# Kernel optimization log

Hardware: AMD Instinct MI355X
Metric: run time of the kernel (lower is better)

The kernel has to match this reference:

```python
import jax, jax.numpy as jnp
import numpy as np

B, N, MAX_V = 256, 16384, 64

def setup_inputs() -> dict:
    key = jax.random.key(0)
    ks = jax.random.split(key, 11)
    s = 0.02
    x = jax.random.normal(ks[0], (B, N, 5), dtype=jnp.float32)
    W1 = jax.random.normal(ks[1], (2, 32), dtype=jnp.float32) * s
    b1 = jnp.zeros((32,), jnp.float32)
    W2 = jax.random.normal(ks[2], (32, 64), dtype=jnp.float32) * s
    b2 = jnp.zeros((64,), jnp.float32)
    W3 = jax.random.normal(ks[3], (201, 256), dtype=jnp.float32) * s
    b3 = jnp.zeros((256,), jnp.float32)
    W4 = jax.random.normal(ks[4], (256, 128), dtype=jnp.float32) * s
    b4 = jnp.zeros((128,), jnp.float32)
    W5 = jax.random.normal(ks[5], (128, MAX_V * 4), dtype=jnp.float32) * s
    # existence-logit biases initialized to -2.0 (indices i*4+3)
    b5 = jnp.zeros((MAX_V * 4,), jnp.float32).at[jnp.arange(MAX_V) * 4 + 3].set(-2.0)
    return {"x": x, "W1": W1, "b1": b1, "W2": W2, "b2": b2,
            "W3": W3, "b3": b3, "W4": W4, "b4": b4, "W5": W5, "b5": b5}

def _pca_align(coords):
    # coords: [B,N,3]
    n = coords.shape[1]
    centroid = coords.mean(axis=1, keepdims=True)          # [B,1,3]
    centered = coords - centroid                           # [B,N,3]
    cov = jnp.einsum('bni,bnj->bij', centered, centered) / n
    evals, evecs = jnp.linalg.eigh(cov)                    # ascending
    evals = evals[:, ::-1]                                 # descending
    evecs = evecs[:, :, ::-1]
    # det sign fix on 3rd column
    det = jnp.linalg.det(evecs)
    evecs = evecs.at[:, :, 2].multiply(jnp.where(det < 0, -1.0, 1.0)[:, None])
    # deterministic sign: each axis points toward side with more mass (vectorized)
    proj = jnp.einsum('bnd,bde->bne', centered, evecs)     # [B,N,3]
    pos = (proj > 0).sum(axis=1)
    neg = (proj < 0).sum(axis=1)
    sign = jnp.where(neg > pos, -1.0, 1.0)                 # [B,3]
    evecs = evecs * sign[:, None, :]
    aligned = jnp.einsum('bnd,bde->bne', centered, evecs)  # [B,N,3]
    eig_norm = evals / (evals.sum(axis=1, keepdims=True) + 1e-8)
    extents = aligned.max(axis=1) - aligned.min(axis=1)    # [B,3]
    pca_features = jnp.concatenate([eig_norm, extents, centroid[:, 0]], axis=1)  # [B,9]
    return aligned, pca_features, evecs, centroid

def reference(x, W1, b1, W2, b2, W3, b3, W4, b4, W5, b5):
    coords = x[:, :, :3]
    sem = x[:, :, 3:]                                      # [B,N,2]
    aligned, pca_features, rot, centroid = _pca_align(coords)
    # per-point MLP
    pf = jax.nn.relu(sem @ W1 + b1)
    pf = jax.nn.relu(pf @ W2 + b2)                         # [B,N,64]
    gmax = pf.max(axis=1)
    gavg = pf.mean(axis=1)
    gstd = jnp.std(pf, axis=1, ddof=1)                     # torch.std is unbiased
    g = jnp.concatenate([gmax, gavg, gstd, pca_features], axis=1)  # [B,201]
    h = jax.nn.relu(g @ W3 + b3)
    h = jax.nn.relu(h @ W4 + b4)
    out = (h @ W5 + b5).reshape(x.shape[0], MAX_V, 4)      # [B,64,4]
    return out
```

## Files before the change

kernel.cpp:

```cpp
#include <hip/hip_runtime.h>
#include <math.h>

#define BATCH 256
#define NPTS  16384
#define TPB   256

#define P1_CHUNKS     8
#define P1_PTS_BLOCK  (NPTS / P1_CHUNKS)
#define P1_ITERS      8

#define P2_CHUNKS     8
#define P2_PTS_BLOCK  (NPTS / P2_CHUNKS)
#define P2_PTS_THREAD (P2_PTS_BLOCK / TPB)

#define R1_STRIDE 256
#define R1_WORDS  (BATCH * R1_STRIDE)
#define R2_OFF    R1_WORDS
#define R2_STRIDE 32
#define R2_WORDS  (BATCH * R2_STRIDE)
#define R3MAX_OFF (R2_OFF + R2_WORDS)
#define R3MIN_OFF (R3MAX_OFF + BATCH * 4)

typedef __bf16 bf16x8 __attribute__((ext_vector_type(8)));
typedef float  floatx4 __attribute__((ext_vector_type(4)));

__device__ __forceinline__ unsigned floatToKey(float f) {
    unsigned u = __float_as_uint(f);
    return (u & 0x80000000u) ? ~u : (u | 0x80000000u);
}
__device__ __forceinline__ float keyToFloat(unsigned k) {
    unsigned u = (k & 0x80000000u) ? (k ^ 0x80000000u) : ~k;
    return __uint_as_float(u);
}

__global__ void init_ws_kernel(unsigned* __restrict__ wsu) {
    int i = blockIdx.x * TPB + threadIdx.x;
    if (i < R1_WORDS) wsu[i] = 0u;
    if (i < BATCH * 4) {
        wsu[R3MAX_OFF + i] = 0u;
        wsu[R3MIN_OFF + i] = 0xFFFFFFFFu;
    }
}

__global__ __launch_bounds__(TPB, 4)
void pass1_kernel(const float* __restrict__ x, const float* __restrict__ W1,
                  const float* __restrict__ b1, const float* __restrict__ W2,
                  const float* __restrict__ b2, float* __restrict__ ws) {
    const int b     = blockIdx.x;
    const int chunk = blockIdx.y;
    const int tid   = threadIdx.x;
    const int lane  = tid & 63;
    const int wave  = tid >> 6;
    const int quad  = lane >> 4;
    const int l15   = lane & 15;

    bf16x8 Bf[4];
    float  b2n[4];
#pragma unroll
    for (int t = 0; t < 4; ++t) {
        int n = t * 16 + l15;
#pragma unroll
        for (int j = 0; j < 8; ++j)
            Bf[t][j] = (__bf16)W2[(quad * 8 + j) * 64 + n];
        b2n[t] = b2[n];
    }
    float w1a[8], w1b[8], b1r[8];
#pragma unroll
    for (int j = 0; j < 8; ++j) {
        int jj = quad * 8 + j;
        w1a[j] = W1[jj];
        w1b[j] = W1[32 + jj];
        b1r[j] = b1[jj];
    }

    float vmax[4] = {0.f, 0.f, 0.f, 0.f};
    float vsum[4] = {0.f, 0.f, 0.f, 0.f};
    float vsq[4]  = {0.f, 0.f, 0.f, 0.f};
    float mo[9];
#pragma unroll
    for (int j = 0; j < 9; ++j) mo[j] = 0.f;

    const float* xb = x + ((size_t)b * NPTS + (size_t)chunk * P1_PTS_BLOCK) * 5;

    for (int it = 0; it < P1_ITERS; ++it) {
        const int pbase = wave * (P1_ITERS * 64) + it * 64;
        const float* p = xb + (size_t)(pbase + lane) * 5;
        float c0 = p[0], c1 = p[1], c2 = p[2], s0 = p[3], s1 = p[4];
        mo[0] += c0; mo[1] += c1; mo[2] += c2;
        mo[3] = fmaf(c0, c0, mo[3]); mo[4] = fmaf(c0, c1, mo[4]); mo[5] = fmaf(c0, c2, mo[5]);
        mo[6] = fmaf(c1, c1, mo[6]); mo[7] = fmaf(c1, c2, mo[7]); mo[8] = fmaf(c1 == c1 ? c2 : c2, c2, mo[8]);

#pragma unroll
        for (int g = 0; g < 4; ++g) {
            int src = g * 16 + l15;
            float gs0 = __shfl(s0, src);
            float gs1 = __shfl(s1, src);
            bf16x8 Af;
#pragma unroll
            for (int j = 0; j < 8; ++j) {
                float v = fmaf(gs0, w1a[j], fmaf(gs1, w1b[j], b1r[j]));
                Af[j] = (__bf16)fmaxf(v, 0.f);
            }
#pragma unroll
            for (int t = 0; t < 4; ++t) {
                floatx4 C = {0.f, 0.f, 0.f, 0.f};
                C = __builtin_amdgcn_mfma_f32_16x16x32_bf16(Af, Bf[t], C, 0, 0, 0);
#pragma unroll
                for (int r = 0; r < 4; ++r) {
                    float v = fmaxf(C[r] + b2n[t], 0.f);
                    vmax[t] = fmaxf(vmax[t], v);
                    vsum[t] += v;
                    vsq[t]  = fmaf(v, v, vsq[t]);
                }
            }
        }
    }

#pragma unroll
    for (int t = 0; t < 4; ++t) {
        vmax[t] = fmaxf(vmax[t], __shfl_xor(vmax[t], 16));
        vmax[t] = fmaxf(vmax[t], __shfl_xor(vmax[t], 32));
        vsum[t] += __shfl_xor(vsum[t], 16);
        vsum[t] += __shfl_xor(vsum[t], 32);
        vsq[t]  += __shfl_xor(vsq[t], 16);
        vsq[t]  += __shfl_xor(vsq[t], 32);
    }
#pragma unroll
    for (int j = 0; j < 9; ++j) {
        float v = mo[j];
#pragma unroll
        for (int o = 32; o > 0; o >>= 1) v += __shfl_xor(v, o);
        mo[j] = v;
    }

    __shared__ float red[4][201];
    if (quad == 0) {
#pragma unroll
        for (int t = 0; t < 4; ++t) {
            red[wave][t * 16 + l15]       = vmax[t];
            red[wave][64 + t * 16 + l15]  = vsum[t];
            red[wave][128 + t * 16 + l15] = vsq[t];
        }
    }
    if (lane == 0) {
#pragma unroll
        for (int j = 0; j < 9; ++j) red[wave][192 + j] = mo[j];
    }
    __syncthreads();

    if (tid < 201) {
        float v0 = red[0][tid], v1 = red[1][tid], v2 = red[2][tid], v3 = red[3][tid];
        float* base = ws + (size_t)b * R1_STRIDE;
        if (tid < 64) {
            float m = fmaxf(fmaxf(v0, v1), fmaxf(v2, v3));
            atomicMax((unsigned*)(base + 9 + tid), __float_as_uint(m));
        } else if (tid < 128) {
            atomicAdd(base + 73 + (tid - 64), v0 + v1 + v2 + v3);
        } else if (tid < 192) {
            atomicAdd(base + 137 + (tid - 128), v0 + v1 + v2 + v3);
        } else {
            atomicAdd(base + (tid - 192), v0 + v1 + v2 + v3);
        }
    }
}

__global__ void eigh_kernel(float* __restrict__ ws) {
    int b = blockIdx.x * blockDim.x + threadIdx.x;
    if (b >= BATCH) return;
    const float* r1 = ws + (size_t)b * R1_STRIDE;
    const double n = (double)NPTS;
    double mx = r1[0] / n, my = r1[1] / n, mz = r1[2] / n;
    double A[3][3];
    A[0][0] = r1[3] / n - mx * mx; A[0][1] = r1[4] / n - mx * my; A[0][2] = r1[5] / n - mx * mz;
    A[1][1] = r1[6] / n - my * my; A[1][2] = r1[7] / n - my * mz; A[2][2] = r1[8] / n - mz * mz;
    A[1][0] = A[0][1]; A[2][0] = A[0][2]; A[2][1] = A[1][2];
    double V[3][3] = {{1, 0, 0}, {0, 1, 0}, {0, 0, 1}};

    const int PP[3] = {0, 0, 1};
    const int QQ[3] = {1, 2, 2};
    for (int sweep = 0; sweep < 12; ++sweep) {
        for (int r3 = 0; r3 < 3; ++r3) {
            int p = PP[r3], q = QQ[r3];
            double apq = A[p][q];
            if (fabs(apq) < 1e-300) continue;
            double theta = (A[q][q] - A[p][p]) / (2.0 * apq);
            double t = 1.0 / (fabs(theta) + sqrt(theta * theta + 1.0));
            if (theta < 0.0) t = -t;
            double c = 1.0 / sqrt(t * t + 1.0), s = t * c;
            double apq_t = t * apq;
            A[p][p] -= apq_t;
            A[q][q] += apq_t;
            A[p][q] = A[q][p] = 0.0;
            for (int r = 0; r < 3; ++r) {
                if (r != p && r != q) {
                    double arp = A[r][p], arq = A[r][q];
                    A[r][p] = A[p][r] = c * arp - s * arq;
                    A[r][q] = A[q][r] = s * arp + c * arq;
                }
                double vrp = V[r][p], vrq = V[r][q];
                V[r][p] = c * vrp - s * vrq;
                V[r][q] = s * vrp + c * vrq;
            }
        }
    }
    double w[3] = {A[0][0], A[1][1], A[2][2]};
    int i0 = 0, i1 = 1, i2 = 2, t;
    if (w[i0] < w[i1]) { t = i0; i0 = i1; i1 = t; }
    if (w[i0] < w[i2]) { t = i0; i0 = i2; i2 = t; }
    if (w[i1] < w[i2]) { t = i1; i1 = i2; i2 = t; }
    int idx[3] = {i0, i1, i2};

    float* r2 = ws + R2_OFF + (size_t)b * R2_STRIDE;
    for (int e = 0; e < 3; ++e)
        for (int comp = 0; comp < 3; ++comp)
            r2[e * 3 + comp] = (float)V[comp][idx[e]];
    double sum = w[0] + w[1] + w[2] + 1e-8;
    for (int e = 0; e < 3; ++e) r2[9 + e] = (float)(w[idx[e]] / sum);
    r2[12] = (float)mx; r2[13] = (float)my; r2[14] = (float)mz;
}

__global__ __launch_bounds__(TPB)
void pass2_kernel(const float* __restrict__ x, float* __restrict__ ws) {
    const int b = blockIdx.x, chunk = blockIdx.y, tid = threadIdx.x;
    const int lane = tid & 63, wave = tid >> 6;
    const float* r2 = ws + R2_OFF + (size_t)b * R2_STRIDE;
    float e0x = r2[0], e0y = r2[1], e0z = r2[2];
    float e1x = r2[3], e1y = r2[4], e1z = r2[5];
    float e2x = r2[6], e2y = r2[7], e2z = r2[8];
    float cx = r2[12], cy = r2[13], cz = r2[14];

    const float* xb = x + ((size_t)b * NPTS + (size_t)chunk * P2_PTS_BLOCK) * 5;
    float mn[3] = {3.4e38f, 3.4e38f, 3.4e38f};
    float mx[3] = {-3.4e38f, -3.4e38f, -3.4e38f};
    for (int i = 0; i < P2_PTS_THREAD; ++i) {
        const float* p = xb + (size_t)(i * TPB + tid) * 5;
        float c0 = p[0] - cx, c1 = p[1] - cy, c2 = p[2] - cz;
        float p0 = fmaf(c0, e0x, fmaf(c1, e0y, c2 * e0z));
        float p1 = fmaf(c0, e1x, fmaf(c1, e1y, c2 * e1z));
        float p2 = fmaf(c0, e2x, fmaf(c1, e2y, c2 * e2z));
        mn[0] = fminf(mn[0], p0); mx[0] = fmaxf(mx[0], p0);
        mn[1] = fminf(mn[1], p1); mx[1] = fmaxf(mx[1], p1);
        mn[2] = fminf(mn[2], p2); mx[2] = fmaxf(mx[2], p2);
    }
    __shared__ float red[4][8];
#pragma unroll
    for (int d = 0; d < 3; ++d) {
        float v = mx[d];
#pragma unroll
        for (int o = 32; o > 0; o >>= 1) v = fmaxf(v, __shfl_xor(v, o));
        if (lane == 0) red[wave][d] = v;
    }
#pragma unroll
    for (int d = 0; d < 3; ++d) {
        float v = mn[d];
#pragma unroll
        for (int o = 32; o > 0; o >>= 1) v = fminf(v, __shfl_xor(v, o));
        if (lane == 0) red[wave][4 + d] = v;
    }
    __syncthreads();
    unsigned* wsu = (unsigned*)ws;
    if (tid < 3) {
        float m = fmaxf(fmaxf(red[0][tid], red[1][tid]), fmaxf(red[2][tid], red[3][tid]));
        atomicMax(&wsu[R3MAX_OFF + b * 4 + tid], floatToKey(m));
    } else if (tid < 6) {
        int d = tid - 3;
        float m = fminf(fminf(red[0][4 + d], red[1][4 + d]), fminf(red[2][4 + d], red[3][4 + d]));
        atomicMin(&wsu[R3MIN_OFF + b * 4 + d], floatToKey(m));
    }
}

__global__ __launch_bounds__(TPB)
void final_kernel(const float* __restrict__ W3, const float* __restrict__ b3,
                  const float* __restrict__ W4, const float* __restrict__ b4,
                  const float* __restrict__ W5, const float* __restrict__ b5,
                  const float* __restrict__ ws, float* __restrict__ out) {
    const int b = blockIdx.x, t = threadIdx.x;
    __shared__ float g[224];
    __shared__ float h1[256];
    __shared__ float h2[128];
    const float* r1 = ws + (size_t)b * R1_STRIDE;
    if (t < 64) {
        g[t] = r1[9 + t];
        float s = r1[73 + t], sq = r1[137 + t];
        float avg = s * (1.0f / NPTS);
        g[64 + t] = avg;
        float var = (sq - s * avg) / (float)(NPTS - 1);
        g[128 + t] = sqrtf(fmaxf(var, 0.f));
    } else if (t < 73) {
        int j = t - 64;
        const float* r2 = ws + R2_OFF + (size_t)b * R2_STRIDE;
        const unsigned* wsu = (const unsigned*)ws;
        if (j < 3) {
            g[192 + j] = r2[9 + j];
        } else if (j < 6) {
            int d = j - 3;
            float fmx = keyToFloat(wsu[R3MAX_OFF + b * 4 + d]);
            float fmn = keyToFloat(wsu[R3MIN_OFF + b * 4 + d]);
            g[195 + d] = fmx - fmn;
        } else {
            g[198 + (j - 6)] = r2[12 + (j - 6)];
        }
    }
    __syncthreads();
    float a = b3[t];
    for (int j = 0; j < 201; ++j) a = fmaf(g[j], W3[j * 256 + t], a);
    h1[t] = fmaxf(a, 0.f);
    __syncthreads();
    if (t < 128) {
        float a2 = b4[t];
        for (int j = 0; j < 256; ++j) a2 = fmaf(h1[j], W4[j * 128 + t], a2);
        h2[t] = fmaxf(a2, 0.f);
    }
    __syncthreads();
    float o = b5[t];
    for (int j = 0; j < 128; ++j) o = fmaf(h2[j], W5[j * 256 + t], o);
    out[(size_t)b * 256 + t] = o;
}

extern "C" void kernel_launch(void* const* d_in, const int* in_sizes, int n_in,
                              void* d_out, int out_size, void* d_ws, size_t ws_size,
                              hipStream_t stream) {
    const float* x  = (const float*)d_in[0];
    const float* W1 = (const float*)d_in[1];
    const float* b1 = (const float*)d_in[2];
    const float* W2 = (const float*)d_in[3];
    const float* b2 = (const float*)d_in[4];
    const float* W3 = (const float*)d_in[5];
    const float* b3 = (const float*)d_in[6];
    const float* W4 = (const float*)d_in[7];
    const float* b4 = (const float*)d_in[8];
    const float* W5 = (const float*)d_in[9];
    const float* b5 = (const float*)d_in[10];
    float* out = (float*)d_out;
    float* ws  = (float*)d_ws;

    init_ws_kernel<<<dim3(R1_WORDS / TPB), TPB, 0, stream>>>((unsigned*)ws);
    pass1_kernel<<<dim3(BATCH, P1_CHUNKS), TPB, 0, stream>>>(x, W1, b1, W2, b2, ws);
    eigh_kernel<<<dim3(4), 64, 0, stream>>>(ws);
    pass2_kernel<<<dim3(BATCH, P2_CHUNKS), TPB, 0, stream>>>(x, ws);
    final_kernel<<<dim3(BATCH), TPB, 0, stream>>>(W3, b3, W4, b4, W5, b5, ws, out);
}
```

Before: 230.9 us.

## Fuse eigh, projection pass and MLP head into one per-batch kernel

Replaces the five-kernel pipeline with two kernels. pass1 now writes per-chunk partials instead of atomics, so the workspace init kernel is no longer needed. A new mid_kernel per batch combines the partials, runs a float Jacobi eigen-solve on one thread (fewer sweeps, down from double), does the min/max projection pass over all points, and runs the MLP head. pass1 also folds bias into the MFMA accumulator and vectorises the stat accumulation. This removes launches, atomics and global round-trips, but the projection pass now runs with only 256 blocks instead of 2048, which cuts parallelism for that memory-bound pass, and the lower-precision eigensolve may change accuracy.

New measurement: 546.5 us. +136.7%, slower.

```diff
diff --git a/kernel.cpp b/kernel.cpp
--- a/kernel.cpp
+++ b/kernel.cpp
@@ -9,38 +9,11 @@
 #define P1_PTS_BLOCK  (NPTS / P1_CHUNKS)
 #define P1_ITERS      8
 
-#define P2_CHUNKS     8
-#define P2_PTS_BLOCK  (NPTS / P2_CHUNKS)
-#define P2_PTS_THREAD (P2_PTS_BLOCK / TPB)
-
-#define R1_STRIDE 256
-#define R1_WORDS  (BATCH * R1_STRIDE)
-#define R2_OFF    R1_WORDS
-#define R2_STRIDE 32
-#define R2_WORDS  (BATCH * R2_STRIDE)
-#define R3MAX_OFF (R2_OFF + R2_WORDS)
-#define R3MIN_OFF (R3MAX_OFF + BATCH * 4)
-
-typedef __bf16 bf16x8 __attribute__((ext_vector_type(8)));
+#define PART_STRIDE 256
+
+typedef __bf16 bf16x8  __attribute__((ext_vector_type(8)));
 typedef float  floatx4 __attribute__((ext_vector_type(4)));
-
-__device__ __forceinline__ unsigned floatToKey(float f) {
-    unsigned u = __float_as_uint(f);
-    return (u & 0x80000000u) ? ~u : (u | 0x80000000u);
-}
-__device__ __forceinline__ float keyToFloat(unsigned k) {
-    unsigned u = (k & 0x80000000u) ? (k ^ 0x80000000u) : ~k;
-    return __uint_as_float(u);
-}
-
-__global__ void init_ws_kernel(unsigned* __restrict__ wsu) {
-    int i = blockIdx.x * TPB + threadIdx.x;
-    if (i < R1_WORDS) wsu[i] = 0u;
-    if (i < BATCH * 4) {
-        wsu[R3MAX_OFF + i] = 0u;
-        wsu[R3MIN_OFF + i] = 0xFFFFFFFFu;
-    }
-}
+typedef float  floatx2 __attribute__((ext_vector_type(2)));
 
 __global__ __launch_bounds__(TPB, 4)
 void pass1_kernel(const float* __restrict__ x, const float* __restrict__ W1,
@@ -73,14 +46,20 @@
         b1r[j] = b1[jj];
     }
 
-    float vmax[4] = {0.f, 0.f, 0.f, 0.f};
-    float vsum[4] = {0.f, 0.f, 0.f, 0.f};
-    float vsq[4]  = {0.f, 0.f, 0.f, 0.f};
+    floatx4 vmax4[4];
+    floatx2 vs01[4], vs23[4], vq01[4], vq23[4];
+#pragma unroll
+    for (int t = 0; t < 4; ++t) {
+        vmax4[t] = (floatx4){0.f, 0.f, 0.f, 0.f};
+        vs01[t] = (floatx2){0.f, 0.f}; vs23[t] = (floatx2){0.f, 0.f};
+        vq01[t] = (floatx2){0.f, 0.f}; vq23[t] = (floatx2){0.f, 0.f};
+    }
     float mo[9];
 #pragma unroll
     for (int j = 0; j < 9; ++j) mo[j] = 0.f;
 
     const float* xb = x + ((size_t)b * NPTS + (size_t)chunk * P1_PTS_BLOCK) * 5;
+    const floatx4 zero4 = {0.f, 0.f, 0.f, 0.f};
 
     for (int it = 0; it < P1_ITERS; ++it) {
         const int pbase = wave * (P1_ITERS * 64) + it * 64;
@@ -88,7 +67,7 @@
         float c0 = p[0], c1 = p[1], c2 = p[2], s0 = p[3], s1 = p[4];
         mo[0] += c0; mo[1] += c1; mo[2] += c2;
         mo[3] = fmaf(c0, c0, mo[3]); mo[4] = fmaf(c0, c1, mo[4]); mo[5] = fmaf(c0, c2, mo[5]);
-        mo[6] = fmaf(c1, c1, mo[6]); mo[7] = fmaf(c1, c2, mo[7]); mo[8] = fmaf(c1 == c1 ? c2 : c2, c2, mo[8]);
+        mo[6] = fmaf(c1, c1, mo[6]); mo[7] = fmaf(c1, c2, mo[7]); mo[8] = fmaf(c2, c2, mo[8]);
 
 #pragma unroll
         for (int g = 0; g < 4; ++g) {
@@ -103,205 +82,204 @@
             }
 #pragma unroll
             for (int t = 0; t < 4; ++t) {
-                floatx4 C = {0.f, 0.f, 0.f, 0.f};
+                floatx4 C = {b2n[t], b2n[t], b2n[t], b2n[t]};
                 C = __builtin_amdgcn_mfma_f32_16x16x32_bf16(Af, Bf[t], C, 0, 0, 0);
-#pragma unroll
-                for (int r = 0; r < 4; ++r) {
-                    float v = fmaxf(C[r] + b2n[t], 0.f);
-                    vmax[t] = fmaxf(vmax[t], v);
-                    vsum[t] += v;
-                    vsq[t]  = fmaf(v, v, vsq[t]);
+                floatx4 v = __builtin_elementwise_max(C, zero4);
+                vmax4[t] = __builtin_elementwise_max(vmax4[t], v);
+                floatx2 a = {v[0], v[1]};
+                floatx2 c = {v[2], v[3]};
+                vs01[t] += a;
+                vs23[t] += c;
+                vq01[t] = __builtin_elementwise_fma(a, a, vq01[t]);
+                vq23[t] = __builtin_elementwise_fma(c, c, vq23[t]);
+            }
+        }
+    }
+
+    float fmx[4], fsm[4], fsq[4];
+#pragma unroll
+    for (int t = 0; t < 4; ++t) {
+        float m = fmaxf(fmaxf(vmax4[t][0], vmax4[t][1]), fmaxf(vmax4[t][2], vmax4[t][3]));
+        m = fmaxf(m, __shfl_xor(m, 16));
+        m = fmaxf(m, __shfl_xor(m, 32));
+        fmx[t] = m;
+        float s = (vs01[t][0] + vs01[t][1]) + (vs23[t][0] + vs23[t][1]);
+        s += __shfl_xor(s, 16);
+        s += __shfl_xor(s, 32);
+        fsm[t] = s;
+        float q = (vq01[t][0] + vq01[t][1]) + (vq23[t][0] + vq23[t][1]);
+        q += __shfl_xor(q, 16);
+        q += __shfl_xor(q, 32);
+        fsq[t] = q;
+    }
+#pragma unroll
+    for (int j = 0; j < 9; ++j) {
+        float v = mo[j];
+#pragma unroll
+        for (int o = 32; o > 0; o >>= 1) v += __shfl_xor(v, o);
+        mo[j] = v;
+    }
+
+    __shared__ float red[4][201];
+    if (quad == 0) {
+#pragma unroll
+        for (int t = 0; t < 4; ++t) {
+            red[wave][t * 16 + l15]       = fmx[t];
+            red[wave][64 + t * 16 + l15]  = fsm[t];
+            red[wave][128 + t * 16 + l15] = fsq[t];
+        }
+    }
+    if (lane == 0) {
+#pragma unroll
+        for (int j = 0; j < 9; ++j) red[wave][192 + j] = mo[j];
+    }
+    __syncthreads();
+
+    if (tid < 201) {
+        float v0 = red[0][tid], v1 = red[1][tid], v2 = red[2][tid], v3 = red[3][tid];
+        float r = (tid < 64) ? fmaxf(fmaxf(v0, v1), fmaxf(v2, v3))
+                             : (v0 + v1) + (v2 + v3);
+        ws[(size_t)(b * P1_CHUNKS + chunk) * PART_STRIDE + tid] = r;
+    }
+}
+
+__global__ __launch_bounds__(TPB)
+void mid_kernel(const float* __restrict__ x,
+                const float* __restrict__ W3, const float* __restrict__ b3,
+                const float* __restrict__ W4, const float* __restrict__ b4,
+                const float* __restrict__ W5, const float* __restrict__ b5,
+                const float* __restrict__ ws, float* __restrict__ out) {
+    const int b = blockIdx.x, t = threadIdx.x;
+    const int lane = t & 63, wave = t >> 6;
+
+    __shared__ float comb[201];
+    __shared__ float eg[15];
+    __shared__ float redmm[4][8];
+    __shared__ float g[224];
+    __shared__ float h1[256];
+    __shared__ float h2[128];
+
+    if (t < 201) {
+        const float* base = ws + (size_t)b * P1_CHUNKS * PART_STRIDE + t;
+        float acc = base[0];
+        if (t < 64) {
+#pragma unroll
+            for (int i = 1; i < P1_CHUNKS; ++i) acc = fmaxf(acc, base[i * PART_STRIDE]);
+        } else {
+#pragma unroll
+            for (int i = 1; i < P1_CHUNKS; ++i) acc += base[i * PART_STRIDE];
+        }
+        comb[t] = acc;
+    }
+    __syncthreads();
+
+    if (t == 0) {
+        const float n = (float)NPTS;
+        float mx = comb[192] / n, my = comb[193] / n, mz = comb[194] / n;
+        float A[3][3];
+        A[0][0] = comb[195] / n - mx * mx; A[0][1] = comb[196] / n - mx * my;
+        A[0][2] = comb[197] / n - mx * mz;
+        A[1][1] = comb[198] / n - my * my; A[1][2] = comb[199] / n - my * mz;
+        A[2][2] = comb[200] / n - mz * mz;
+        A[1][0] = A[0][1]; A[2][0] = A[0][2]; A[2][1] = A[1][2];
+        float V[3][3] = {{1, 0, 0}, {0, 1, 0}, {0, 0, 1}};
+        const int PP[3] = {0, 0, 1};
+        const int QQ[3] = {1, 2, 2};
+        for (int sweep = 0; sweep < 7; ++sweep) {
+            for (int r3 = 0; r3 < 3; ++r3) {
+                int p = PP[r3], q = QQ[r3];
+                float apq = A[p][q];
+                if (fabsf(apq) < 1e-35f) continue;
+                float theta = (A[q][q] - A[p][p]) / (2.0f * apq);
+                float tt = 1.0f / (fabsf(theta) + sqrtf(fmaf(theta, theta, 1.0f)));
+                if (theta < 0.0f) tt = -tt;
+                float c = 1.0f / sqrtf(fmaf(tt, tt, 1.0f)), s = tt * c;
+                float apq_t = tt * apq;
+                A[p][p] -= apq_t;
+                A[q][q] += apq_t;
+                A[p][q] = A[q][p] = 0.0f;
+                for (int r = 0; r < 3; ++r) {
+                    if (r != p && r != q) {
+                        float arp = A[r][p], arq = A[r][q];
+                        A[r][p] = A[p][r] = c * arp - s * arq;
+                        A[r][q] = A[q][r] = s * arp + c * arq;
+                    }
+                    float vrp = V[r][p], vrq = V[r][q];
+                    V[r][p] = c * vrp - s * vrq;
+                    V[r][q] = s * vrp + c * vrq;
                 }
             }
         }
-    }
-
-#pragma unroll
-    for (int t = 0; t < 4; ++t) {
-        vmax[t] = fmaxf(vmax[t], __shfl_xor(vmax[t], 16));
-        vmax[t] = fmaxf(vmax[t], __shfl_xor(vmax[t], 32));
-        vsum[t] += __shfl_xor(vsum[t], 16);
-        vsum[t] += __shfl_xor(vsum[t], 32);
-        vsq[t]  += __shfl_xor(vsq[t], 16);
-        vsq[t]  += __shfl_xor(vsq[t], 32);
-    }
-#pragma unroll
-    for (int j = 0; j < 9; ++j) {
-        float v = mo[j];
-#pragma unroll
-        for (int o = 32; o > 0; o >>= 1) v += __shfl_xor(v, o);
-        mo[j] = v;
-    }
-
-    __shared__ float red[4][201];
-    if (quad == 0) {
-#pragma unroll
-        for (int t = 0; t < 4; ++t) {
-            red[wave][t * 16 + l15]       = vmax[t];
-            red[wave][64 + t * 16 + l15]  = vsum[t];
-            red[wave][128 + t * 16 + l15] = vsq[t];
-        }
-    }
-    if (lane == 0) {
-#pragma unroll
-        for (int j = 0; j < 9; ++j) red[wave][192 + j] = mo[j];
-    }
-    __syncthreads();
-
-    if (tid < 201) {
-        float v0 = red[0][tid], v1 = red[1][tid], v2 = red[2][tid], v3 = red[3][tid];
-        float* base = ws + (size_t)b * R1_STRIDE;
-        if (tid < 64) {
-            float m = fmaxf(fmaxf(v0, v1), fmaxf(v2, v3));
-            atomicMax((unsigned*)(base + 9 + tid), __float_as_uint(m));
-        } else if (tid < 128) {
-            atomicAdd(base + 73 + (tid - 64), v0 + v1 + v2 + v3);
-        } else if (tid < 192) {
-            atomicAdd(base + 137 + (tid - 128), v0 + v1 + v2 + v3);
-        } else {
-            atomicAdd(base + (tid - 192), v0 + v1 + v2 + v3);
-        }
-    }
-}
-
-__global__ void eigh_kernel(float* __restrict__ ws) {
-    int b = blockIdx.x * blockDim.x + threadIdx.x;
-    if (b >= BATCH) return;
-    const float* r1 = ws + (size_t)b * R1_STRIDE;
-    const double n = (double)NPTS;
-    double mx = r1[0] / n, my = r1[1] / n, mz = r1[2] / n;
-    double A[3][3];
-    A[0][0] = r1[3] / n - mx * mx; A[0][1] = r1[4] / n - mx * my; A[0][2] = r1[5] / n - mx * mz;
-    A[1][1] = r1[6] / n - my * my; A[1][2] = r1[7] / n - my * mz; A[2][2] = r1[8] / n - mz * mz;
-    A[1][0] = A[0][1]; A[2][0] = A[0][2]; A[2][1] = A[1][2];
-    double V[3][3] = {{1, 0, 0}, {0, 1, 0}, {0, 0, 1}};
-
-    const int PP[3] = {0, 0, 1};
-    const int QQ[3] = {1, 2, 2};
-    for (int sweep = 0; sweep < 12; ++sweep) {
-        for (int r3 = 0; r3 < 3; ++r3) {
-            int p = PP[r3], q = QQ[r3];
-            double apq = A[p][q];
-            if (fabs(apq) < 1e-300) continue;
-            double theta = (A[q][q] - A[p][p]) / (2.0 * apq);
-            double t = 1.0 / (fabs(theta) + sqrt(theta * theta + 1.0));
-            if (theta < 0.0) t = -t;
-            double c = 1.0 / sqrt(t * t + 1.0), s = t * c;
-            double apq_t = t * apq;
-            A[p][p] -= apq_t;
-            A[q][q] += apq_t;
-            A[p][q] = A[q][p] = 0.0;
-            for (int r = 0; r < 3; ++r) {
-                if (r != p && r != q) {
-                    double arp = A[r][p], arq = A[r][q];
-                    A[r][p] = A[p][r] = c * arp - s * arq;
-                    A[r][q] = A[q][r] = s * arp + c * arq;
-                }
-                double vrp = V[r][p], vrq = V[r][q];
-                V[r][p] = c * vrp - s * vrq;
-                V[r][q] = s * vrp + c * vrq;
-            }
-        }
-    }
-    double w[3] = {A[0][0], A[1][1], A[2][2]};
-    int i0 = 0, i1 = 1, i2 = 2, t;
-    if (w[i0] < w[i1]) { t = i0; i0 = i1; i1 = t; }
-    if (w[i0] < w[i2]) { t = i0; i0 = i2; i2 = t; }
-    if (w[i1] < w[i2]) { t = i1; i1 = i2; i2 = t; }
-    int idx[3] = {i0, i1, i2};
-
-    float* r2 = ws + R2_OFF + (size_t)b * R2_STRIDE;
-    for (int e = 0; e < 3; ++e)
-        for (int comp = 0; comp < 3; ++comp)
-            r2[e * 3 + comp] = (float)V[comp][idx[e]];
-    double sum = w[0] + w[1] + w[2] + 1e-8;
-    for (int e = 0; e < 3; ++e) r2[9 + e] = (float)(w[idx[e]] / sum);
-    r2[12] = (float)mx; r2[13] = (float)my; r2[14] = (float)mz;
-}
-
-__global__ __launch_bounds__(TPB)
-void pass2_kernel(const float* __restrict__ x, float* __restrict__ ws) {
-    const int b = blockIdx.x, chunk = blockIdx.y, tid = threadIdx.x;
-    const int lane = tid & 63, wave = tid >> 6;
-    const float* r2 = ws + R2_OFF + (size_t)b * R2_STRIDE;
-    float e0x = r2[0], e0y = r2[1], e0z = r2[2];
-    float e1x = r2[3], e1y = r2[4], e1z = r2[5];
-    float e2x = r2[6], e2y = r2[7], e2z = r2[8];
-    float cx = r2[12], cy = r2[13], cz = r2[14];
-
-    const float* xb = x + ((size_t)b * NPTS + (size_t)chunk * P2_PTS_BLOCK) * 5;
+        float w[3] = {A[0][0], A[1][1], A[2][2]};
+        int i0 = 0, i1 = 1, i2 = 2, sw;
+        if (w[i0] < w[i1]) { sw = i0; i0 = i1; i1 = sw; }
+        if (w[i0] < w[i2]) { sw = i0; i0 = i2; i2 = sw; }
+        if (w[i1] < w[i2]) { sw = i1; i1 = i2; i2 = sw; }
+        int idx[3] = {i0, i1, i2};
+        for (int e = 0; e < 3; ++e)
+            for (int comp = 0; comp < 3; ++comp)
+                eg[e * 3 + comp] = V[comp][idx[e]];
+        float sum = w[0] + w[1] + w[2] + 1e-8f;
+        for (int e = 0; e < 3; ++e) eg[9 + e] = w[idx[e]] / sum;
+        eg[12] = mx; eg[13] = my; eg[14] = mz;
+    }
+    __syncthreads();
+
+    float e0x = eg[0], e0y = eg[1], e0z = eg[2];
+    float e1x = eg[3], e1y = eg[4], e1z = eg[5];
+    float e2x = eg[6], e2y = eg[7], e2z = eg[8];
+    float cx = eg[12], cy = eg[13], cz = eg[14];
+
+    const float* xb = x + (size_t)b * NPTS * 5;
     float mn[3] = {3.4e38f, 3.4e38f, 3.4e38f};
-    float mx[3] = {-3.4e38f, -3.4e38f, -3.4e38f};
-    for (int i = 0; i < P2_PTS_THREAD; ++i) {
-        const float* p = xb + (size_t)(i * TPB + tid) * 5;
+    float mx3[3] = {-3.4e38f, -3.4e38f, -3.4e38f};
+#pragma unroll 4
+    for (int i = 0; i < NPTS / TPB; ++i) {
+        const float* p = xb + (size_t)(i * TPB + t) * 5;
         float c0 = p[0] - cx, c1 = p[1] - cy, c2 = p[2] - cz;
         float p0 = fmaf(c0, e0x, fmaf(c1, e0y, c2 * e0z));
         float p1 = fmaf(c0, e1x, fmaf(c1, e1y, c2 * e1z));
         float p2 = fmaf(c0, e2x, fmaf(c1, e2y, c2 * e2z));
-        mn[0] = fminf(mn[0], p0); mx[0] = fmaxf(mx[0], p0);
-        mn[1] = fminf(mn[1], p1); mx[1] = fmaxf(mx[1], p1);
-        mn[2] = fminf(mn[2], p2); mx[2] = fmaxf(mx[2], p2);
-    }
-    __shared__ float red[4][8];
+        mn[0] = fminf(mn[0], p0); mx3[0] = fmaxf(mx3[0], p0);
+        mn[1] = fminf(mn[1], p1); mx3[1] = fmaxf(mx3[1], p1);
+        mn[2] = fminf(mn[2], p2); mx3[2] = fmaxf(mx3[2], p2);
+    }
 #pragma unroll
     for (int d = 0; d < 3; ++d) {
-        float v = mx[d];
+        float v = mx3[d];
 #pragma unroll
         for (int o = 32; o > 0; o >>= 1) v = fmaxf(v, __shfl_xor(v, o));
-        if (lane == 0) red[wave][d] = v;
-    }
-#pragma unroll
-    for (int d = 0; d < 3; ++d) {
-        float v = mn[d];
-#pragma unroll
-        for (int o = 32; o > 0; o >>= 1) v = fminf(v, __shfl_xor(v, o));
-        if (lane == 0) red[wave][4 + d] = v;
-    }
-    __syncthreads();
-    unsigned* wsu = (unsigned*)ws;
-    if (tid < 3) {
-        float m = fmaxf(fmaxf(red[0][tid], red[1][tid]), fmaxf(red[2][tid], red[3][tid]));
-        atomicMax(&wsu[R3MAX_OFF + b * 4 + tid], floatToKey(m));
-    } else if (tid < 6) {
-        int d = tid - 3;
-        float m = fminf(fminf(red[0][4 + d], red[1][4 + d]), fminf(red[2][4 + d], red[3][4 + d]));
-        atomicMin(&wsu[R3MIN_OFF + b * 4 + d], floatToKey(m));
-    }
-}
-
-__global__ __launch_bounds__(TPB)
-void final_kernel(const float* __restrict__ W3, const float* __restrict__ b3,
-                  const float* __restrict__ W4, const float* __restrict__ b4,
-                  const float* __restrict__ W5, const float* __restrict__ b5,
-                  const float* __restrict__ ws, float* __restrict__ out) {
-    const int b = blockIdx.x, t = threadIdx.x;
-    __shared__ float g[224];
-    __shared__ float h1[256];
-    __shared__ float h2[128];
-    const float* r1 = ws + (size_t)b * R1_STRIDE;
+        if (lane == 0) redmm[wave][d] = v;
+        float u = mn[d];
+#pragma unroll
+        for (int o = 32; o > 0; o >>= 1) u = fminf(u, __shfl_xor(u, o));
+        if (lane == 0) redmm[wave][4 + d] = u;
+    }
+    __syncthreads();
+
     if (t < 64) {
-        g[t] = r1[9 + t];
-        float s = r1[73 + t], sq = r1[137 + t];
+        g[t] = comb[t];
+        float s = comb[64 + t], sq = comb[128 + t];
         float avg = s * (1.0f / NPTS);
         g[64 + t] = avg;
         float var = (sq - s * avg) / (float)(NPTS - 1);
         g[128 + t] = sqrtf(fmaxf(var, 0.f));
     } else if (t < 73) {
         int j = t - 64;
-        const float* r2 = ws + R2_OFF + (size_t)b * R2_STRIDE;
-        const unsigned* wsu = (const unsigned*)ws;
         if (j < 3) {
-            g[192 + j] = r2[9 + j];
+            g[192 + j] = eg[9 + j];
         } else if (j < 6) {
             int d = j - 3;
-            float fmx = keyToFloat(wsu[R3MAX_OFF + b * 4 + d]);
-            float fmn = keyToFloat(wsu[R3MIN_OFF + b * 4 + d]);
+            float fmx = fmaxf(fmaxf(redmm[0][d], redmm[1][d]), fmaxf(redmm[2][d], redmm[3][d]));
+            float fmn = fminf(fminf(redmm[0][4 + d], redmm[1][4 + d]),
+                              fminf(redmm[2][4 + d], redmm[3][4 + d]));
             g[195 + d] = fmx - fmn;
         } else {
-            g[198 + (j - 6)] = r2[12 + (j - 6)];
-        }
-    }
-    __syncthreads();
+            g[198 + (j - 6)] = eg[12 + (j - 6)];
+        }
+    }
+    __syncthreads();
+
     float a = b3[t];
     for (int j = 0; j < 201; ++j) a = fmaf(g[j], W3[j * 256 + t], a);
     h1[t] = fmaxf(a, 0.f);
@@ -334,9 +312,6 @@
     float* out = (float*)d_out;
     float* ws  = (float*)d_ws;
 
-    init_ws_kernel<<<dim3(R1_WORDS / TPB), TPB, 0, stream>>>((unsigned*)ws);
     pass1_kernel<<<dim3(BATCH, P1_CHUNKS), TPB, 0, stream>>>(x, W1, b1, W2, b2, ws);
-    eigh_kernel<<<dim3(4), 64, 0, stream>>>(ws);
-    pass2_kernel<<<dim3(BATCH, P2_CHUNKS), TPB, 0, stream>>>(x, ws);
-    final_kernel<<<dim3(BATCH), TPB, 0, stream>>>(W3, b3, W4, b4, W5, b5, ws, out);
+    mid_kernel<<<dim3(BATCH), TPB, 0, stream>>>(x, W3, b3, W4, b4, W5, b5, ws, out);
 }
```
